# Kernel tuning notes

Measured on AMD Instinct MI355X. Metric: run time of the kernel, lower is better.

The kernel has to match this reference:

```python
import jax, jax.numpy as jnp
import numpy as np


def _window_indices(L, K):
    # 0-based (emo, cau) index pairs kept in the torch flattening order:
    # emo varies slowly (outer), cau varies fast (inner), |cau-emo| <= K.
    i = np.repeat(np.arange(L), L)
    j = np.tile(np.arange(L), L)
    m = np.abs(j - i) <= K
    return i[m], j[m]


def setup_inputs() -> dict:
    key = jax.random.key(0)
    ks = jax.random.split(key, 6)
    B, L, D = 4, 512, 768
    K, P = 10, 50
    R = 2 * D + P  # rank_feat_dim = 1586
    return {
        "doc_sents_h": jax.random.normal(ks[0], (B, L, D), jnp.float32),
        "pos_emb": jax.random.normal(ks[1], (2 * K + 1, P), jnp.float32) * 0.05,
        "W1": jax.random.normal(ks[2], (R, R), jnp.float32) * (1.0 / np.sqrt(R)),
        "b1": jax.random.normal(ks[3], (R,), jnp.float32) * 0.01,
        "W2": jax.random.normal(ks[4], (R, 1), jnp.float32) * (1.0 / np.sqrt(R)),
        "b2": jax.random.normal(ks[5], (1,), jnp.float32) * 0.01,
    }


def reference(doc_sents_h, pos_emb, W1, b1, W2, b2):
    B, L, D = doc_sents_h.shape
    K = (pos_emb.shape[0] - 1) // 2
    ei, ci = _window_indices(L, K)           # static numpy, shape [n]
    rel = jnp.asarray(ci - ei)               # [n] in [-K, K]
    # windowed pair features, [B, n, 2D] (skips the O(L^2) materialization)
    P_pairs = jnp.concatenate([doc_sents_h[:, ei], doc_sents_h[:, ci]], axis=-1)
    emb = pos_emb[rel + K]                   # [n, pos_dim]
    relf = rel.astype(pos_emb.dtype)
    kernel = jnp.exp(-jnp.square(relf[:, None] - relf[None, :]))  # [n, n]
    emb = kernel @ emb                       # [n, pos_dim], batch-invariant
    couples = jnp.concatenate(
        [P_pairs, jnp.broadcast_to(emb, (B,) + emb.shape)], axis=-1)  # [B, n, R]
    h = jax.nn.relu(couples @ W1 + b1)       # [B, n, R]
    pred = (h @ W2 + b2)[..., 0]             # [B, n]
    emo_cau_pos = jnp.stack(
        [jnp.asarray(ei) + 1, jnp.asarray(ci) + 1], axis=1)  # [n, 2], 1-based
    return pred, emo_cau_pos, h
```

## Files before the change

kernel.cpp:

```cpp
#include <hip/hip_runtime.h>
#include <math.h>

#define B_   4
#define L_   512
#define D_   768
#define K_   10
#define P_   50
#define R_   1586
#define NP_  10642
#define MROWS 2048
#define NPAD 1664
#define UVS  1600

#define PRED_OFF 0
#define POS_OFF  (B_ * NP_)
#define H_OFF    (B_ * NP_ + NP_ * 2)

typedef __attribute__((ext_vector_type(8))) short short8;
typedef __attribute__((ext_vector_type(4))) float floatx4;

__device__ __forceinline__ unsigned short f2bf(float f) {
    union { float f; unsigned int u; } a; a.f = f;
    unsigned int u = a.u;
    return (unsigned short)((u + 0x7FFF + ((u >> 16) & 1)) >> 16);
}
__device__ __forceinline__ float bf2f(unsigned short u) {
    union { unsigned int u; float f; } a; a.u = ((unsigned int)u) << 16;
    return a.f;
}

__device__ __forceinline__ int pair_offset(int i) {
    int h = i < K_ ? i : K_;
    int off = h * (K_ + 1) + (h * (h - 1)) / 2;
    if (i > K_) {
        int fullEnd = i < (L_ - K_) ? i : (L_ - K_);
        off += (fullEnd - K_) * (2 * K_ + 1);
        if (i > L_ - K_) {
            int t = i - (L_ - K_);
            int first = 2 * K_;
            int last = L_ + K_ - (i - 1);
            off += (first + last) * t / 2;
        }
    }
    return off;
}

#define CA_BLOCKS 1536
#define CW_BLOCKS 2496
__global__ __launch_bounds__(256) void prep(
        const float* __restrict__ doc, const float* __restrict__ pos_emb,
        const float* __restrict__ W1, const float* __restrict__ b1,
        unsigned short* __restrict__ At, unsigned short* __restrict__ Wt,
        unsigned short* __restrict__ Fb) {
    __shared__ float tile[32][33];
    __shared__ float Es[P_];
    const int bid = blockIdx.x;

    if (bid < CA_BLOCKS) {
        int idx = (bid * 256 + threadIdx.x) * 4;
        float4 v = *(const float4*)(doc + idx);
        ushort4 o;
        o.x = f2bf(v.x); o.y = f2bf(v.y); o.z = f2bf(v.z); o.w = f2bf(v.w);
        *(ushort4*)(At + idx) = o;
        return;
    }
    if (bid < CA_BLOCKS + CW_BLOCKS) {
        int bb = bid - CA_BLOCKS;
        int z = bb / 1248, rem = bb % 1248;
        int k0 = (rem % 24) * 32;
        int n0 = (rem / 24) * 32;
        int tx = threadIdx.x & 31, ty = threadIdx.x >> 5;
        #pragma unroll
        for (int r = 0; r < 4; ++r) {
            int k = k0 + ty + r * 8;
            int n = n0 + tx;
            tile[ty + r * 8][tx] = (n < R_) ? W1[(size_t)(z * D_ + k) * R_ + n] : 0.f;
        }
        __syncthreads();
        #pragma unroll
        for (int r = 0; r < 4; ++r) {
            int n = n0 + ty + r * 8;
            int k = k0 + tx;
            Wt[(size_t)z * NPAD * D_ + (size_t)n * D_ + k] = f2bf(tile[tx][ty + r * 8]);
        }
        return;
    }
    int s = bid - (CA_BLOCKS + CW_BLOCKS);
    if (threadIdx.x < P_) {
        float acc = 0.f;
        #pragma unroll
        for (int r = 0; r <= 2 * K_; ++r) {
            float cnt = (float)(L_ - (r > K_ ? r - K_ : K_ - r));
            float d = (float)(s - r);
            acc += cnt * expf(-d * d) * pos_emb[r * P_ + threadIdx.x];
        }
        Es[threadIdx.x] = acc;
    }
    __syncthreads();
    for (int j = threadIdx.x; j < R_; j += 256) {
        float acc = b1[j];
        #pragma unroll 10
        for (int p = 0; p < P_; ++p)
            acc += Es[p] * W1[(2 * D_ + p) * R_ + j];
        Fb[s * UVS + j] = f2bf(acc);
    }
}

#define GLOAD_LDS16(g, l) __builtin_amdgcn_global_load_lds( \
    (const __attribute__((address_space(1))) void*)(g), \
    (__attribute__((address_space(3))) void*)(l), 16, 0, 0)

__global__ __launch_bounds__(256) void gemm_mfma(
        const unsigned short* __restrict__ At,
        const unsigned short* __restrict__ Wt,
        unsigned short* __restrict__ U, unsigned short* __restrict__ V) {
    __shared__ unsigned short Alds[2][128 * 32];
    __shared__ unsigned short Blds[2][128 * 32];
    const int tileN = blockIdx.x * 128;
    const int tileM = blockIdx.y * 128;
    const unsigned short* Bt = Wt + (size_t)blockIdx.z * NPAD * D_;
    unsigned short* C = blockIdx.z ? V : U;

    const int lane = threadIdx.x & 63;
    const int w = threadIdx.x >> 6;
    const int wm = (w & 1) * 64, wn = (w >> 1) * 64;
    const int quad = lane >> 4, l16 = lane & 15;

    floatx4 acc[4][4] = {};

#define STAGE(buf, kk) do { \
        _Pragma("unroll") \
        for (int t = 0; t < 2; ++t) { \
            int g = (t * 4 + w) * 64 + lane; \
            int m = g >> 2, c = g & 3; \
            GLOAD_LDS16(At + (size_t)(tileM + m) * D_ + (kk) + c * 8, \
                        &Alds[buf][(t * 4 + w) * 512]); \
            GLOAD_LDS16(Bt + (size_t)(tileN + m) * D_ + (kk) + c * 8, \
                        &Blds[buf][(t * 4 + w) * 512]); \
        } } while (0)

#define KSTEP(rb, kk, dopf) do { \
        if (dopf) { \
            STAGE(rb ^ 1, (kk) + 32); \
            asm volatile("s_waitcnt vmcnt(4)" ::: "memory"); \
        } else { \
            asm volatile("s_waitcnt vmcnt(0)" ::: "memory"); \
        } \
        __builtin_amdgcn_s_barrier(); \
        __builtin_amdgcn_sched_barrier(0); \
        short8 a[4], b[4]; \
        _Pragma("unroll") \
        for (int im = 0; im < 4; ++im) \
            a[im] = *(const short8*)&Alds[rb][(wm + im * 16 + l16) * 32 + quad * 8]; \
        _Pragma("unroll") \
        for (int in = 0; in < 4; ++in) \
            b[in] = *(const short8*)&Blds[rb][(wn + in * 16 + l16) * 32 + quad * 8]; \
        _Pragma("unroll") \
        for (int im = 0; im < 4; ++im) \
            _Pragma("unroll") \
            for (int in = 0; in < 4; ++in) \
                acc[im][in] = __builtin_amdgcn_mfma_f32_16x16x32_bf16( \
                    a[im], b[in], acc[im][in], 0, 0, 0); \
        __builtin_amdgcn_sched_barrier(0); \
        __builtin_amdgcn_s_barrier(); \
    } while (0)

    STAGE(0, 0);
    for (int k0 = 0; k0 < D_; k0 += 64) {
        KSTEP(0, k0, true);
        KSTEP(1, k0 + 32, (k0 + 64) < D_);
    }
#undef KSTEP
#undef STAGE

    #pragma unroll
    for (int im = 0; im < 4; ++im) {
        #pragma unroll
        for (int in = 0; in < 4; ++in) {
            int col = tileN + wn + in * 16 + l16;
            if (col < R_) {
                #pragma unroll
                for (int r = 0; r < 4; ++r) {
                    int row = tileM + wm + im * 16 + quad * 4 + r;
                    C[(size_t)row * UVS + col] = f2bf(acc[im][in][r]);
                }
            }
        }
    }
}

#define NC2 13
__global__ __launch_bounds__(256) void epilogue(
        const unsigned short* __restrict__ U, const unsigned short* __restrict__ V,
        const unsigned short* __restrict__ Fb, const float* __restrict__ W2,
        const float* __restrict__ b2, float* __restrict__ out) {
    const int w    = threadIdx.x >> 6;
    const int lane = threadIdx.x & 63;
    const int b    = blockIdx.x >> 9;
    const int i    = blockIdx.x & (L_ - 1);

    const ushort2* u2  = (const ushort2*)(U + (size_t)(b * L_ + i) * UVS);
    const float2*  w2v = (const float2*)W2;

    float2 ur[NC2], wr[NC2];
    #pragma unroll
    for (int t = 0; t < NC2; ++t) {
        int c = lane + t * 64;
        if (c < R_ / 2) {
            ushort2 uu = u2[c];
            ur[t] = make_float2(bf2f(uu.x), bf2f(uu.y));
            wr[t] = w2v[c];
        }
    }

    const int base = i - K_ > 0 ? i - K_ : 0;
    const int poff = pair_offset(i);
    const float bias = b2[0];

    for (int dj = w; dj < 2 * K_ + 1; dj += 4) {
        int j = i - K_ + dj;
        if ((unsigned)j >= L_) continue;
        int p = poff + (j - base);
        const ushort2* v2 = (const ushort2*)(V + (size_t)(b * L_ + j) * UVS);
        const ushort2* f2 = (const ushort2*)(Fb + (size_t)dj * UVS);
        double* h2 = (double*)(out + H_OFF + (size_t)(b * NP_ + p) * R_);

        float acc = 0.f;
        #pragma unroll
        for (int t = 0; t < NC2; ++t) {
            int c = lane + t * 64;
            if (c < R_ / 2) {
                ushort2 vv = v2[c], ff = f2[c];
                float h0 = fmaxf(ur[t].x + bf2f(vv.x) + bf2f(ff.x), 0.f);
                float h1 = fmaxf(ur[t].y + bf2f(vv.y) + bf2f(ff.y), 0.f);
                union { float2 f; double d; } pk;
                pk.f = make_float2(h0, h1);
                __builtin_nontemporal_store(pk.d, h2 + c);
                acc += h0 * wr[t].x + h1 * wr[t].y;
            }
        }
        #pragma unroll
        for (int off = 32; off; off >>= 1) acc += __shfl_down(acc, off, 64);
        if (lane == 0) {
            out[PRED_OFF + b * NP_ + p] = acc + bias;
            if (b == 0) {
                out[POS_OFF + p * 2 + 0] = (float)(i + 1);
                out[POS_OFF + p * 2 + 1] = (float)(j + 1);
            }
        }
    }
}

extern "C" void kernel_launch(void* const* d_in, const int* in_sizes, int n_in,
                              void* d_out, int out_size, void* d_ws, size_t ws_size,
                              hipStream_t stream) {
    const float* doc     = (const float*)d_in[0];
    const float* pos_emb = (const float*)d_in[1];
    const float* W1      = (const float*)d_in[2];
    const float* b1      = (const float*)d_in[3];
    const float* W2      = (const float*)d_in[4];
    const float* b2      = (const float*)d_in[5];
    float* out = (float*)d_out;

    char* ws = (char*)d_ws;
    size_t off = 0;
    unsigned short* U  = (unsigned short*)(ws + off); off += (size_t)MROWS * UVS * 2;
    unsigned short* V  = (unsigned short*)(ws + off); off += (size_t)MROWS * UVS * 2;
    unsigned short* Fb = (unsigned short*)(ws + off); off += (size_t)21 * UVS * 2;
    off = (off + 255) & ~(size_t)255;
    unsigned short* At = (unsigned short*)(ws + off); off += (size_t)MROWS * D_ * 2;
    off = (off + 255) & ~(size_t)255;
    unsigned short* Wt = (unsigned short*)(ws + off);

    prep<<<CA_BLOCKS + CW_BLOCKS + 21, 256, 0, stream>>>(
        doc, pos_emb, W1, b1, At, Wt, Fb);
    gemm_mfma<<<dim3(NPAD / 128, MROWS / 128, 2), 256, 0, stream>>>(At, Wt, U, V);
    epilogue<<<dim3(MROWS), 256, 0, stream>>>(U, V, Fb, W2, b2, out);
}
```

Baseline: 363.6 us.

## Deepen GEMM K-tile to 64 with XOR-swizzled LDS and vectorize epilogue loads

```diff
diff --git a/kernel.cpp b/kernel.cpp
--- a/kernel.cpp
+++ b/kernel.cpp
@@ -114,8 +114,8 @@
         const unsigned short* __restrict__ At,
         const unsigned short* __restrict__ Wt,
         unsigned short* __restrict__ U, unsigned short* __restrict__ V) {
-    __shared__ unsigned short Alds[2][128 * 32];
-    __shared__ unsigned short Blds[2][128 * 32];
+    __shared__ unsigned short Alds[2][128 * 64];
+    __shared__ unsigned short Blds[2][128 * 64];
     const int tileN = blockIdx.x * 128;
     const int tileM = blockIdx.y * 128;
     const unsigned short* Bt = Wt + (size_t)blockIdx.z * NPAD * D_;
@@ -130,45 +130,56 @@
 
 #define STAGE(buf, kk) do { \
         _Pragma("unroll") \
-        for (int t = 0; t < 2; ++t) { \
-            int g = (t * 4 + w) * 64 + lane; \
-            int m = g >> 2, c = g & 3; \
-            GLOAD_LDS16(At + (size_t)(tileM + m) * D_ + (kk) + c * 8, \
-                        &Alds[buf][(t * 4 + w) * 512]); \
-            GLOAD_LDS16(Bt + (size_t)(tileN + m) * D_ + (kk) + c * 8, \
-                        &Blds[buf][(t * 4 + w) * 512]); \
+        for (int t = 0; t < 4; ++t) { \
+            int chunk = t * 4 + w;                \
+            int r = chunk * 8 + (lane >> 3); \
+            int sl = (lane & 7) ^ (lane >> 3);    \
+            GLOAD_LDS16(At + (size_t)(tileM + r) * D_ + (kk) + sl * 8, \
+                        &Alds[buf][chunk * 512]); \
+            GLOAD_LDS16(Bt + (size_t)(tileN + r) * D_ + (kk) + sl * 8, \
+                        &Blds[buf][chunk * 512]); \
         } } while (0)
 
 #define KSTEP(rb, kk, dopf) do { \
         if (dopf) { \
-            STAGE(rb ^ 1, (kk) + 32); \
-            asm volatile("s_waitcnt vmcnt(4)" ::: "memory"); \
+            STAGE(rb ^ 1, (kk) + 64); \
+            asm volatile("s_waitcnt vmcnt(8)" ::: "memory"); \
         } else { \
             asm volatile("s_waitcnt vmcnt(0)" ::: "memory"); \
         } \
         __builtin_amdgcn_s_barrier(); \
         __builtin_amdgcn_sched_barrier(0); \
-        short8 a[4], b[4]; \
+        short8 a[4][2], b[4][2]; \
         _Pragma("unroll") \
         for (int im = 0; im < 4; ++im) \
-            a[im] = *(const short8*)&Alds[rb][(wm + im * 16 + l16) * 32 + quad * 8]; \
+            _Pragma("unroll") \
+            for (int ks = 0; ks < 2; ++ks) \
+                a[im][ks] = *(const short8*)&Alds[rb][ \
+                    (wm + im * 16 + l16) * 64 + \
+                    (((ks * 4 + quad) ^ (l16 & 7)) * 8)]; \
         _Pragma("unroll") \
         for (int in = 0; in < 4; ++in) \
-            b[in] = *(const short8*)&Blds[rb][(wn + in * 16 + l16) * 32 + quad * 8]; \
+            _Pragma("unroll") \
+            for (int ks = 0; ks < 2; ++ks) \
+                b[in][ks] = *(const short8*)&Blds[rb][ \
+                    (wn + in * 16 + l16) * 64 + \
+                    (((ks * 4 + quad) ^ (l16 & 7)) * 8)]; \
         _Pragma("unroll") \
         for (int im = 0; im < 4; ++im) \
             _Pragma("unroll") \
             for (int in = 0; in < 4; ++in) \
-                acc[im][in] = __builtin_amdgcn_mfma_f32_16x16x32_bf16( \
-                    a[im], b[in], acc[im][in], 0, 0, 0); \
+                _Pragma("unroll") \
+                for (int ks = 0; ks < 2; ++ks) \
+                    acc[im][in] = __builtin_amdgcn_mfma_f32_16x16x32_bf16( \
+                        a[im][ks], b[in][ks], acc[im][in], 0, 0, 0); \
         __builtin_amdgcn_sched_barrier(0); \
         __builtin_amdgcn_s_barrier(); \
     } while (0)
 
     STAGE(0, 0);
-    for (int k0 = 0; k0 < D_; k0 += 64) {
+    for (int k0 = 0; k0 < D_; k0 += 128) {
         KSTEP(0, k0, true);
-        KSTEP(1, k0 + 32, (k0 + 64) < D_);
+        KSTEP(1, k0 + 64, (k0 + 128) < D_);
     }
 #undef KSTEP
 #undef STAGE
@@ -189,7 +200,7 @@
     }
 }
 
-#define NC2 13
+#define NG 4
 __global__ __launch_bounds__(256) void epilogue(
         const unsigned short* __restrict__ U, const unsigned short* __restrict__ V,
         const unsigned short* __restrict__ Fb, const float* __restrict__ W2,
@@ -199,17 +210,25 @@
     const int b    = blockIdx.x >> 9;
     const int i    = blockIdx.x & (L_ - 1);
 
-    const ushort2* u2  = (const ushort2*)(U + (size_t)(b * L_ + i) * UVS);
-    const float2*  w2v = (const float2*)W2;
-
-    float2 ur[NC2], wr[NC2];
+    const unsigned short* urow = U + (size_t)(b * L_ + i) * UVS;
+
+    float uf[NG][8], wf[NG][8];
     #pragma unroll
-    for (int t = 0; t < NC2; ++t) {
+    for (int t = 0; t < NG; ++t) {
         int c = lane + t * 64;
-        if (c < R_ / 2) {
-            ushort2 uu = u2[c];
-            ur[t] = make_float2(bf2f(uu.x), bf2f(uu.y));
-            wr[t] = w2v[c];
+        if (c < 198) {
+            short8 uu = *(const short8*)(urow + 8 * c);
+            float4 wa = *(const float4*)(W2 + 8 * c);
+            float4 wb = *(const float4*)(W2 + 8 * c + 4);
+            #pragma unroll
+            for (int e = 0; e < 8; ++e) uf[t][e] = bf2f((unsigned short)uu[e]);
+            wf[t][0] = wa.x; wf[t][1] = wa.y; wf[t][2] = wa.z; wf[t][3] = wa.w;
+            wf[t][4] = wb.x; wf[t][5] = wb.y; wf[t][6] = wb.z; wf[t][7] = wb.w;
+        } else if (c == 198) {
+            ushort2 uu = *(const ushort2*)(urow + 1584);
+            float2 wt = *(const float2*)(W2 + 1584);
+            uf[t][0] = bf2f(uu.x); uf[t][1] = bf2f(uu.y);
+            wf[t][0] = wt.x;       wf[t][1] = wt.y;
         }
     }
 
@@ -221,22 +240,34 @@
         int j = i - K_ + dj;
         if ((unsigned)j >= L_) continue;
         int p = poff + (j - base);
-        const ushort2* v2 = (const ushort2*)(V + (size_t)(b * L_ + j) * UVS);
-        const ushort2* f2 = (const ushort2*)(Fb + (size_t)dj * UVS);
-        double* h2 = (double*)(out + H_OFF + (size_t)(b * NP_ + p) * R_);
+        const unsigned short* vrow = V + (size_t)(b * L_ + j) * UVS;
+        const unsigned short* frow = Fb + (size_t)dj * UVS;
+        float2* h2 = (float2*)(out + H_OFF + (size_t)(b * NP_ + p) * R_);
 
         float acc = 0.f;
         #pragma unroll
-        for (int t = 0; t < NC2; ++t) {
+        for (int t = 0; t < NG; ++t) {
             int c = lane + t * 64;
-            if (c < R_ / 2) {
-                ushort2 vv = v2[c], ff = f2[c];
-                float h0 = fmaxf(ur[t].x + bf2f(vv.x) + bf2f(ff.x), 0.f);
-                float h1 = fmaxf(ur[t].y + bf2f(vv.y) + bf2f(ff.y), 0.f);
-                union { float2 f; double d; } pk;
-                pk.f = make_float2(h0, h1);
-                __builtin_nontemporal_store(pk.d, h2 + c);
-                acc += h0 * wr[t].x + h1 * wr[t].y;
+            if (c < 198) {
+                short8 vv = *(const short8*)(vrow + 8 * c);
+                short8 ff = *(const short8*)(frow + 8 * c);
+                float h[8];
+                #pragma unroll
+                for (int e = 0; e < 8; ++e) {
+                    h[e] = fmaxf(uf[t][e] + bf2f((unsigned short)vv[e])
+                                          + bf2f((unsigned short)ff[e]), 0.f);
+                    acc += h[e] * wf[t][e];
+                }
+                #pragma unroll
+                for (int q = 0; q < 4; ++q)
+                    h2[4 * c + q] = make_float2(h[2 * q], h[2 * q + 1]);
+            } else if (c == 198) {
+                ushort2 vv = *(const ushort2*)(vrow + 1584);
+                ushort2 ff = *(const ushort2*)(frow + 1584);
+                float h0 = fmaxf(uf[t][0] + bf2f(vv.x) + bf2f(ff.x), 0.f);
+                float h1 = fmaxf(uf[t][1] + bf2f(vv.y) + bf2f(ff.y), 0.f);
+                h2[792] = make_float2(h0, h1);
+                acc += h0 * wf[t][0] + h1 * wf[t][1];
             }
         }
         #pragma unroll
```

Result: slower. 376.1 us (+3.4%).
